# Kernel tuning notes

Measured on AMD Instinct MI355X. Metric: run time of the kernel, lower is better.

## Reference

```python
import jax, jax.numpy as jnp
import numpy as np

N = 50000
NEG_SLOPE = 0.2


def leaky_relu(x, slope=NEG_SLOPE):
    return jnp.where(x >= 0, x, slope * x)


def gat_conv(x, edge_index, W, a_src, a_dst, bias):
    """PyG GATConv, heads=1, add_self_loops=True.
    x: [N, Fin], edge_index: [2, E] (row 0 = source j, row 1 = target i),
    W: [Fin, Fout], a_src/a_dst: [Fout], bias: [Fout].
    """
    n = x.shape[0]
    # add self loops
    loops = jnp.arange(n, dtype=edge_index.dtype)
    src = jnp.concatenate([edge_index[0], loops])
    dst = jnp.concatenate([edge_index[1], loops])

    xw = x @ W                       # [N, Fout]
    alpha_src = xw @ a_src           # [N]
    alpha_dst = xw @ a_dst           # [N]

    e = leaky_relu(alpha_src[src] + alpha_dst[dst])   # [E+N]
    # segment softmax over edges sharing the same target node
    m = jax.ops.segment_max(e, dst, num_segments=n)   # [N]
    ex = jnp.exp(e - m[dst])
    denom = jax.ops.segment_sum(ex, dst, num_segments=n)  # [N] (>0 via self loops)
    att = ex / denom[dst]                              # [E+N]

    msgs = att[:, None] * xw[src]                      # [E+N, Fout]
    out = jax.ops.segment_sum(msgs, dst, num_segments=n)
    return out + bias


def setup_inputs() -> dict:
    key = jax.random.key(0)
    ks = jax.random.split(key, 12)
    E = 800000
    Fin, H, Fout = 128, 256, 128
    x = jax.random.normal(ks[0], (N, Fin), dtype=jnp.float32)
    edge_index = jax.random.randint(ks[1], (2, E), 0, N, dtype=jnp.int64)
    s = 0.1
    W1 = jax.random.normal(ks[2], (Fin, H), dtype=jnp.float32) * s
    a1_src = jax.random.normal(ks[3], (H,), dtype=jnp.float32) * s
    a1_dst = jax.random.normal(ks[4], (H,), dtype=jnp.float32) * s
    b1 = jax.random.normal(ks[5], (H,), dtype=jnp.float32) * s
    W2 = jax.random.normal(ks[6], (H, Fout), dtype=jnp.float32) * s
    a2_src = jax.random.normal(ks[7], (Fout,), dtype=jnp.float32) * s
    a2_dst = jax.random.normal(ks[8], (Fout,), dtype=jnp.float32) * s
    b2 = jax.random.normal(ks[9], (Fout,), dtype=jnp.float32) * s
    return {"x": x, "edge_index": edge_index, "W1": W1, "a1_src": a1_src,
            "a1_dst": a1_dst, "b1": b1, "W2": W2, "a2_src": a2_src,
            "a2_dst": a2_dst, "b2": b2}


def reference(x, edge_index, W1, a1_src, a1_dst, b1, W2, a2_src, a2_dst, b2):
    h = jax.nn.relu(gat_conv(x, edge_index, W1, a1_src, a1_dst, b1))
    return gat_conv(h, edge_index, W2, a2_src, a2_dst, b2)
```

## Files before the change

kernel.cpp:

```cpp
#include <hip/hip_runtime.h>
#include <hip/hip_bf16.h>

typedef __attribute__((ext_vector_type(8))) short short8;
typedef __attribute__((ext_vector_type(4))) float floatx4;

#define CAP 8192
#define BIN_CH 2048

__device__ __forceinline__ float read_f(const void* p, long long i, int fp32m) {
  return fp32m ? ((const float*)p)[i] : (float)((const __hip_bfloat16*)p)[i];
}
__device__ __forceinline__ float bf2f(unsigned short u) {
  return __uint_as_float((unsigned)u << 16);
}
__device__ __forceinline__ unsigned short f2bf(float f) {
  const unsigned u = __float_as_uint(f);
  return (unsigned short)((u + 0x7fffu + ((u >> 16) & 1u)) >> 16);
}

__device__ __forceinline__ void pack_one(const void* W, unsigned short* Wp, int i,
                                         int K, int NOUT, int m) {
  const int k = i / NOUT, n = i - k * NOUT;
  const int ct = n >> 4, c = n & 15, ks = k >> 5, quad = (k >> 3) & 3, j = k & 7;
  Wp[(((ct * (K / 32) + ks) * 4 + quad) * 16 + c) * 8 + j] = f2bf(read_f(W, i, m));
}

__global__ __launch_bounds__(256) void prep_k(const void* __restrict__ x,
                                              const void* __restrict__ ei,
                                              const void* __restrict__ W1,
                                              const void* __restrict__ a1s,
                                              const void* __restrict__ a1d,
                                              const void* __restrict__ b1,
                                              const void* __restrict__ W2,
                                              const void* __restrict__ a2s,
                                              const void* __restrict__ a2d,
                                              const void* __restrict__ b2,
                                              unsigned short* __restrict__ Wp1,
                                              unsigned short* __restrict__ Wp2,
                                              float* __restrict__ w_as1, float* __restrict__ w_ad1,
                                              float* __restrict__ v_a2s, float* __restrict__ v_a2d,
                                              float* __restrict__ v_b1,  float* __restrict__ v_b2,
                                              int* __restrict__ bkcnt,
                                              int* __restrict__ flags) {
  __shared__ int fl_s[2];
  const int t = threadIdx.x, b = blockIdx.x;
  if (t < 64) {
    const unsigned short w = ((const unsigned short*)x)[t * 2];
    const int ef = (w >> 7) & 0xff;
    const bool bf_ok = (ef >= 90 && ef <= 140);
    const unsigned hi = ((const unsigned*)ei)[t * 2 + 1];
    const unsigned long long bm = __ballot(bf_ok);
    const unsigned long long zm = __ballot(hi == 0u);
    if (t == 0) {
      fl_s[0] = (bm == ~0ull) ? 0 : 1;
      fl_s[1] = (zm == ~0ull) ? 1 : 0;
      if (b == 0) { flags[0] = fl_s[0]; flags[1] = fl_s[1]; }
    }
  }
  __syncthreads();
  const int m = fl_s[0];

  if (b < 128) {
    pack_one(W1, Wp1, b * 256 + t, 128, 256, m);
  } else if (b < 256) {
    pack_one(W2, Wp2, (b - 128) * 256 + t, 256, 128, m);
  } else if (b == 256) {
    if (t < 128) {
      float sa = 0.f, sb = 0.f;
      for (int j = 0; j < 256; ++j) {
        const float w = read_f(W1, (long long)t * 256 + j, m);
        sa = fmaf(w, read_f(a1s, j, m), sa);
        sb = fmaf(w, read_f(a1d, j, m), sb);
      }
      w_as1[t] = sa;
      w_ad1[t] = sb;
    }
  } else if (b == 257) {
    if (t < 128) v_a2s[t] = read_f(a2s, t, m);
    else         v_a2d[t - 128] = read_f(a2d, t - 128, m);
  } else if (b == 258) {
    v_b1[t] = read_f(b1, t, m);
  } else {
    if (t < 128) v_b2[t] = read_f(b2, t, m);
    bkcnt[t] = 0;
  }
}

__global__ __launch_bounds__(256) void canon_alpha_k(const void* __restrict__ x,
                                                     const float* __restrict__ was,
                                                     const float* __restrict__ wad,
                                                     unsigned short* __restrict__ xb,
                                                     float* __restrict__ as_, float* __restrict__ ad_,
                                                     int n, const int* __restrict__ flags) {
  const int gid = blockIdx.x * 256 + threadIdx.x;
  const int node = gid >> 6, lane = gid & 63;
  if (node >= n) return;
  const int m = flags[0];
  const long long base = (long long)node * 128 + lane * 2;
  const float v0 = read_f(x, base, m), v1 = read_f(x, base + 1, m);
  ushort2 q;
  q.x = f2bf(v0); q.y = f2bf(v1);
  *(ushort2*)(xb + base) = q;
  float s1 = fmaf(v0, was[lane * 2], v1 * was[lane * 2 + 1]);
  float s2 = fmaf(v0, wad[lane * 2], v1 * wad[lane * 2 + 1]);
  for (int off = 32; off; off >>= 1) {
    s1 += __shfl_down(s1, off);
    s2 += __shfl_down(s2, off);
  }
  if (lane == 0) { as_[node] = s1; ad_[node] = s2; }
}

__device__ __forceinline__ void edge_sd(const void* ei, int e, int E, int i64m, int n,
                                        int& s, int& d) {
  if (e < E) {
    if (i64m) { s = (int)((const long long*)ei)[e]; d = (int)((const long long*)ei)[E + e]; }
    else      { s = ((const int*)ei)[e];            d = ((const int*)ei)[E + e]; }
  } else { s = d = e - E; }
  s = min(max(s, 0), n - 1);
  d = min(max(d, 0), n - 1);
}

__global__ __launch_bounds__(256) void bin_k(const void* __restrict__ ei,
                                             unsigned* __restrict__ bpool,
                                             int* __restrict__ bkcnt,
                                             int E, int EN, int n,
                                             const int* __restrict__ flags) {
  __shared__ unsigned stage[BIN_CH];
  __shared__ unsigned daddr[BIN_CH];
  __shared__ int bcnt_s[256], boff_s[256], gbase_s[256], sd[256];
  __shared__ int vtot_s;
  const int t = threadIdx.x;
  const int c0 = blockIdx.x * BIN_CH;
  const int i64m = flags[1];
  bcnt_s[t] = 0;
  __syncthreads();

  unsigned val[BIN_CH / 256];
  int buk[BIN_CH / 256];
#pragma unroll
  for (int i = 0; i < BIN_CH / 256; ++i) {
    const int e = c0 + i * 256 + t;
    if (e < EN) {
      int s, d;
      edge_sd(ei, e, E, i64m, n, s, d);
      buk[i] = d >> 8;
      val[i] = (unsigned)s | ((unsigned)(d & 255) << 16);
      atomicAdd(&bcnt_s[buk[i]], 1);
    } else buk[i] = -1;
  }
  __syncthreads();

  const int c = bcnt_s[t];
  sd[t] = c;
  __syncthreads();
  for (int off = 1; off < 256; off <<= 1) {
    const int v = (t >= off) ? sd[t - off] : 0;
    __syncthreads();
    sd[t] += v;
    __syncthreads();
  }
  boff_s[t] = sd[t] - c;
  if (t == 255) vtot_s = sd[255];
  gbase_s[t] = (c > 0) ? atomicAdd(&bkcnt[t], c) : 0;
  bcnt_s[t] = 0;
  __syncthreads();

#pragma unroll
  for (int i = 0; i < BIN_CH / 256; ++i) {
    if (buk[i] >= 0) {
      const int lp = atomicAdd(&bcnt_s[buk[i]], 1);
      const int si = boff_s[buk[i]] + lp;
      stage[si] = val[i];
      const int gp = gbase_s[buk[i]] + lp;
      daddr[si] = (gp < CAP) ? (unsigned)(buk[i] * CAP + gp) : 0xFFFFFFFFu;
    }
  }
  __syncthreads();

  const int vt = vtot_s;
  for (int idx = t; idx < vt; idx += 256)
    if (daddr[idx] != 0xFFFFFFFFu) bpool[daddr[idx]] = stage[idx];
}

__global__ __launch_bounds__(256) void bucket_csr_k(const unsigned* __restrict__ bpool,
                                                    const int* __restrict__ bkcnt,
                                                    unsigned short* __restrict__ csrc,
                                                    int* __restrict__ start_g,
                                                    int* __restrict__ deg_g, int n) {
  __shared__ int deg_s[256], cur_s[256], sd[256];
  const int t = threadIdx.x, b = blockIdx.x;
  int cnt = bkcnt[b];
  if (cnt > CAP) cnt = CAP;
  deg_s[t] = 0;
  __syncthreads();
  for (int idx = t; idx < cnt; idx += 256) {
    const unsigned v = bpool[b * CAP + idx];
    atomicAdd(&deg_s[(v >> 16) & 255], 1);
  }
  __syncthreads();
  const int dg = deg_s[t];
  sd[t] = dg;
  __syncthreads();
  for (int off = 1; off < 256; off <<= 1) {
    const int v = (t >= off) ? sd[t - off] : 0;
    __syncthreads();
    sd[t] += v;
    __syncthreads();
  }
  const int excl = sd[t] - dg;
  const int node = b * 256 + t;
  if (node < n) { start_g[node] = b * CAP + excl; deg_g[node] = dg; }
  cur_s[t] = excl;
  __syncthreads();
  for (int idx = t; idx < cnt; idx += 256) {
    const unsigned v = bpool[b * CAP + idx];
    const int p = atomicAdd(&cur_s[(v >> 16) & 255], 1);
    csrc[b * CAP + p] = (unsigned short)(v & 0xFFFFu);
  }
}

__device__ __forceinline__ void agg_node(const int start, const int end,
                                         const unsigned short* __restrict__ csrc,
                                         const float* __restrict__ as_, const float adv,
                                         const unsigned short* __restrict__ xw,
                                         const int lane, float* acc) {
  const int slot = lane >> 4, col = lane & 15;
  float dsum = 0.f;
#pragma unroll
  for (int c = 0; c < 8; ++c) acc[c] = 0.f;

  for (int base = start; base < end; base += 64) {
    const int idx = base + lane;
    int s_pre = 0;
    float w_pre = 0.f;
    if (idx < end) {
      s_pre = (int)csrc[idx];
      float v = as_[s_pre] + adv;
      v = (v >= 0.f) ? v : 0.2f * v;
      w_pre = __expf(fminf(v, 60.f));
    }
    dsum += w_pre;
    const int cnt = min(64, end - base);
    for (int j = 0; j < cnt; j += 8) {
      const int jj0 = j + slot, jj1 = j + 4 + slot;
      int s0 = __shfl(s_pre, jj0);
      float w0 = __shfl(w_pre, jj0);
      int s1 = __shfl(s_pre, jj1);
      float w1 = __shfl(w_pre, jj1);
      const bool ok0 = (jj0 < cnt), ok1 = (jj1 < cnt);
      s0 = ok0 ? s0 : 0; w0 = ok0 ? w0 : 0.f;
      s1 = ok1 ? s1 : 0; w1 = ok1 ? w1 : 0.f;
      const short8 q0 = *(const short8*)(xw + (size_t)s0 * 128 + col * 8);
      const short8 q1 = *(const short8*)(xw + (size_t)s1 * 128 + col * 8);
#pragma unroll
      for (int c = 0; c < 8; ++c) {
        acc[c] = fmaf(w0, bf2f((unsigned short)q0[c]), acc[c]);
        acc[c] = fmaf(w1, bf2f((unsigned short)q1[c]), acc[c]);
      }
    }
  }
  for (int off = 32; off; off >>= 1) dsum += __shfl_down(dsum, off);
  dsum = __shfl(dsum, 0);
  const float r = 1.f / fmaxf(dsum, 1e-30f);
#pragma unroll
  for (int c = 0; c < 8; ++c) {
    acc[c] += __shfl_xor(acc[c], 16);
    acc[c] += __shfl_xor(acc[c], 32);
    acc[c] *= r;
  }
}

#define LSTR 136
#define HSTR 264
__global__ __launch_bounds__(1024) void agg_gemm12_k(const int* __restrict__ start_g,
                                                     const int* __restrict__ deg_g,
                                                     const unsigned short* __restrict__ csrc,
                                                     const float* __restrict__ as_,
                                                     const float* __restrict__ ad_,
                                                     const unsigned short* __restrict__ xb,
                                                     const unsigned short* __restrict__ Wp1,
                                                     const unsigned short* __restrict__ Wp2,
                                                     const float* __restrict__ v_b1,
                                                     const float* __restrict__ v_a2s,
                                                     const float* __restrict__ v_a2d,
                                                     unsigned short* __restrict__ xw2,
                                                     float* __restrict__ as2,
                                                     float* __restrict__ ad2, int n) {
  __shared__ unsigned short lds[16 * LSTR];
  __shared__ unsigned short hs[16 * HSTR];
  __shared__ float al_s[16], al_d[16];
  const int wv = threadIdx.x >> 6, lane = threadIdx.x & 63;
  const int slot = lane >> 4, col = lane & 15;
  const int node = blockIdx.x * 16 + wv;

  float acc[8];
  if (node < n) {
    const int start = start_g[node];
    agg_node(start, start + deg_g[node], csrc, as_, ad_[node], xb, lane, acc);
  } else {
#pragma unroll
    for (int c = 0; c < 8; ++c) acc[c] = 0.f;
  }
  if (slot == 0) {
    short8 q;
#pragma unroll
    for (int c = 0; c < 8; ++c) q[c] = (short)f2bf(acc[c]);
    *(short8*)&lds[wv * LSTR + col * 8] = q;
  }
  __syncthreads();

  const int quad = slot, c = col;
  floatx4 g = {0.f, 0.f, 0.f, 0.f};
#pragma unroll
  for (int ks = 0; ks < 4; ++ks) {
    const short8 af = *(const short8*)&lds[c * LSTR + ks * 32 + quad * 8];
    const short8 bf = *(const short8*)(Wp1 + (size_t)((wv * 4 + ks) * 64 + lane) * 8);
    g = __builtin_amdgcn_mfma_f32_16x16x32_bf16(af, bf, g, 0, 0, 0);
  }
  const float bv = v_b1[wv * 16 + c];
#pragma unroll
  for (int r = 0; r < 4; ++r) {
    const float v = g[r] + bv;
    hs[(quad * 4 + r) * HSTR + wv * 16 + c] = f2bf(v > 0.f ? v : 0.f);
  }
  if (threadIdx.x < 16) { al_s[threadIdx.x] = 0.f; al_d[threadIdx.x] = 0.f; }
  __syncthreads();

  const int row0 = blockIdx.x * 16;
  if (wv < 8) {
    floatx4 a2 = {0.f, 0.f, 0.f, 0.f};
#pragma unroll
    for (int ks = 0; ks < 8; ++ks) {
      const short8 af = *(const short8*)&hs[c * HSTR + ks * 32 + quad * 8];
      const short8 bf = *(const short8*)(Wp2 + (size_t)((wv * 8 + ks) * 64 + lane) * 8);
      a2 = __builtin_amdgcn_mfma_f32_16x16x32_bf16(af, bf, a2, 0, 0, 0);
    }
    const float asv = v_a2s[wv * 16 + c], adv = v_a2d[wv * 16 + c];
    float pa_s[4], pa_d[4];
#pragma unroll
    for (int r = 0; r < 4; ++r) {
      pa_s[r] = a2[r] * asv;
      pa_d[r] = a2[r] * adv;
      const int rr = row0 + quad * 4 + r;
      if (rr < n) xw2[(size_t)rr * 128 + wv * 16 + c] = f2bf(a2[r]);
    }
    for (int off = 1; off < 16; off <<= 1) {
#pragma unroll
      for (int r = 0; r < 4; ++r) {
        pa_s[r] += __shfl_xor(pa_s[r], off);
        pa_d[r] += __shfl_xor(pa_d[r], off);
      }
    }
    if (c == 0) {
#pragma unroll
      for (int r = 0; r < 4; ++r) {
        atomicAdd(&al_s[quad * 4 + r], pa_s[r]);
        atomicAdd(&al_d[quad * 4 + r], pa_d[r]);
      }
    }
  }
  __syncthreads();
  if (threadIdx.x < 16) {
    const int rr = row0 + threadIdx.x;
    if (rr < n) { as2[rr] = al_s[threadIdx.x]; ad2[rr] = al_d[threadIdx.x]; }
  }
}

__global__ __launch_bounds__(256) void agg_out_k(const int* __restrict__ start_g,
                                                 const int* __restrict__ deg_g,
                                                 const unsigned short* __restrict__ csrc,
                                                 const float* __restrict__ as_,
                                                 const float* __restrict__ ad_,
                                                 const unsigned short* __restrict__ xw,
                                                 const float* __restrict__ bias,
                                                 void* __restrict__ outp, int n,
                                                 const int* __restrict__ flags) {
  const int gid = blockIdx.x * 256 + threadIdx.x;
  const int node = gid >> 6, lane = gid & 63;
  if (node >= n) return;
  const int slot = lane >> 4, col = lane & 15;
  const int start = start_g[node];
  float acc[8];
  agg_node(start, start + deg_g[node], csrc, as_, ad_[node], xw, lane, acc);
  if (slot == 0) {
    const int c0 = col * 8;
    if (flags[0]) {
      float* o = (float*)outp + (size_t)node * 128 + c0;
      floatx4 q0, q1;
#pragma unroll
      for (int c = 0; c < 4; ++c) {
        q0[c] = acc[c] + bias[c0 + c];
        q1[c] = acc[c + 4] + bias[c0 + 4 + c];
      }
      *(floatx4*)o = q0;
      *(floatx4*)(o + 4) = q1;
    } else {
      short8 q;
#pragma unroll
      for (int c = 0; c < 8; ++c) q[c] = (short)f2bf(acc[c] + bias[c0 + c]);
      *(short8*)((unsigned short*)outp + (size_t)node * 128 + c0) = q;
    }
  }
}

extern "C" void kernel_launch(void* const* d_in, const int* in_sizes, int n_in,
                              void* d_out, int out_size, void* d_ws, size_t ws_size,
                              hipStream_t stream) {
  const void* x   = d_in[0];
  const void* ei  = d_in[1];
  const void* W1  = d_in[2];
  const void* a1s = d_in[3];
  const void* a1d = d_in[4];
  const void* b1  = d_in[5];
  const void* W2  = d_in[6];
  const void* a2s = d_in[7];
  const void* a2d = d_in[8];
  const void* b2  = d_in[9];

  const int N  = in_sizes[0] / 128;
  const int E  = in_sizes[1] / 2;
  const int EN = E + N;
  const int NBUK = (N + 255) / 256;

  unsigned short* B1 = (unsigned short*)d_ws;
  unsigned short* H  = B1 + (size_t)N * 128;
  unsigned short* xw2 = H;
  float* as2 = (float*)(H + (size_t)N * 128);
  float* ad2 = as2 + N;
  float* as_   = (float*)(H + (size_t)N * 256);
  float* ad_   = as_ + N;
  int*   start_g = (int*)(ad_ + N);
  int*   deg_g   = start_g + N;
  int*   bkcnt   = deg_g + N;
  unsigned* bpool = (unsigned*)(bkcnt + 256);
  unsigned short* csrc = (unsigned short*)(bpool + (size_t)NBUK * CAP);
  unsigned short* Wp1 = csrc + (size_t)NBUK * CAP;
  unsigned short* Wp2 = Wp1 + 128 * 256;
  float* vecs  = (float*)(Wp2 + 256 * 128);
  int*   flags = (int*)(vecs + 1152);
  float* w_as1 = vecs,        *w_ad1 = vecs + 128;
  float* v_a2s = vecs + 256,  *v_a2d = vecs + 384;
  float* v_b1  = vecs + 512,  *v_b2  = vecs + 768;

  const int NB = (N * 64 + 255) / 256;
  const int BB = (EN + BIN_CH - 1) / BIN_CH;
  const int AG = (N + 15) / 16;

  prep_k<<<260, 256, 0, stream>>>(x, ei, W1, a1s, a1d, b1, W2, a2s, a2d, b2,
                                  Wp1, Wp2, w_as1, w_ad1, v_a2s, v_a2d, v_b1, v_b2,
                                  bkcnt, flags);

  canon_alpha_k<<<NB, 256, 0, stream>>>(x, w_as1, w_ad1, B1, as_, ad_, N, flags);

  bin_k<<<BB, 256, 0, stream>>>(ei, bpool, bkcnt, E, EN, N, flags);
  bucket_csr_k<<<NBUK, 256, 0, stream>>>(bpool, bkcnt, csrc, start_g, deg_g, N);

  agg_gemm12_k<<<AG, 1024, 0, stream>>>(start_g, deg_g, csrc, as_, ad_, B1, Wp1, Wp2,
                                        v_b1, v_a2s, v_a2d, xw2, as2, ad2, N);

  agg_out_k<<<NB, 256, 0, stream>>>(start_g, deg_g, csrc, as2, ad2, xw2, v_b2, d_out, N, flags);
}
```

Measured before the change: 256.7 us.

## Fuse canon/alpha and edge binning launches, unroll gather, swizzle LDS tiles

Merges the x-canonicalisation/alpha kernel and the edge binning kernel into one launch whose blocks split by index. Each block recomputes the dtype flags from the inputs instead of reading them from prep. The aggregation gather loop now handles 16 neighbours per iteration, giving four independent row loads in flight. The padded LDS strides in the fused GEMM kernel are replaced by XOR swizzling to avoid bank conflicts. The heuristic dtype detection could misclassify inputs.

Result: slower. 278.7 us (+8.6%).

```diff
diff --git a/kernel.cpp b/kernel.cpp
--- a/kernel.cpp
+++ b/kernel.cpp
@@ -86,30 +86,6 @@
   }
 }
 
-__global__ __launch_bounds__(256) void canon_alpha_k(const void* __restrict__ x,
-                                                     const float* __restrict__ was,
-                                                     const float* __restrict__ wad,
-                                                     unsigned short* __restrict__ xb,
-                                                     float* __restrict__ as_, float* __restrict__ ad_,
-                                                     int n, const int* __restrict__ flags) {
-  const int gid = blockIdx.x * 256 + threadIdx.x;
-  const int node = gid >> 6, lane = gid & 63;
-  if (node >= n) return;
-  const int m = flags[0];
-  const long long base = (long long)node * 128 + lane * 2;
-  const float v0 = read_f(x, base, m), v1 = read_f(x, base + 1, m);
-  ushort2 q;
-  q.x = f2bf(v0); q.y = f2bf(v1);
-  *(ushort2*)(xb + base) = q;
-  float s1 = fmaf(v0, was[lane * 2], v1 * was[lane * 2 + 1]);
-  float s2 = fmaf(v0, wad[lane * 2], v1 * wad[lane * 2 + 1]);
-  for (int off = 32; off; off >>= 1) {
-    s1 += __shfl_down(s1, off);
-    s2 += __shfl_down(s2, off);
-  }
-  if (lane == 0) { as_[node] = s1; ad_[node] = s2; }
-}
-
 __device__ __forceinline__ void edge_sd(const void* ei, int e, int E, int i64m, int n,
                                         int& s, int& d) {
   if (e < E) {
@@ -120,66 +96,105 @@
   d = min(max(d, 0), n - 1);
 }
 
-__global__ __launch_bounds__(256) void bin_k(const void* __restrict__ ei,
-                                             unsigned* __restrict__ bpool,
-                                             int* __restrict__ bkcnt,
-                                             int E, int EN, int n,
-                                             const int* __restrict__ flags) {
+__global__ __launch_bounds__(256) void front2_k(const void* __restrict__ x,
+                                                const void* __restrict__ ei,
+                                                const float* __restrict__ w_as1,
+                                                const float* __restrict__ w_ad1,
+                                                unsigned short* __restrict__ xb,
+                                                float* __restrict__ as_, float* __restrict__ ad_,
+                                                unsigned* __restrict__ bpool,
+                                                int* __restrict__ bkcnt,
+                                                int n, int E, int EN, int nbc) {
+  __shared__ int fl_s[2];
   __shared__ unsigned stage[BIN_CH];
   __shared__ unsigned daddr[BIN_CH];
-  __shared__ int bcnt_s[256], boff_s[256], gbase_s[256], sd[256];
+  __shared__ int shA[256], shB[256], shC[256], shD[256];
   __shared__ int vtot_s;
-  const int t = threadIdx.x;
-  const int c0 = blockIdx.x * BIN_CH;
-  const int i64m = flags[1];
-  bcnt_s[t] = 0;
-  __syncthreads();
-
-  unsigned val[BIN_CH / 256];
-  int buk[BIN_CH / 256];
-#pragma unroll
-  for (int i = 0; i < BIN_CH / 256; ++i) {
-    const int e = c0 + i * 256 + t;
-    if (e < EN) {
-      int s, d;
-      edge_sd(ei, e, E, i64m, n, s, d);
-      buk[i] = d >> 8;
-      val[i] = (unsigned)s | ((unsigned)(d & 255) << 16);
-      atomicAdd(&bcnt_s[buk[i]], 1);
-    } else buk[i] = -1;
-  }
-  __syncthreads();
-
-  const int c = bcnt_s[t];
-  sd[t] = c;
-  __syncthreads();
-  for (int off = 1; off < 256; off <<= 1) {
-    const int v = (t >= off) ? sd[t - off] : 0;
-    __syncthreads();
-    sd[t] += v;
-    __syncthreads();
-  }
-  boff_s[t] = sd[t] - c;
-  if (t == 255) vtot_s = sd[255];
-  gbase_s[t] = (c > 0) ? atomicAdd(&bkcnt[t], c) : 0;
-  bcnt_s[t] = 0;
-  __syncthreads();
-
-#pragma unroll
-  for (int i = 0; i < BIN_CH / 256; ++i) {
-    if (buk[i] >= 0) {
-      const int lp = atomicAdd(&bcnt_s[buk[i]], 1);
-      const int si = boff_s[buk[i]] + lp;
-      stage[si] = val[i];
-      const int gp = gbase_s[buk[i]] + lp;
-      daddr[si] = (gp < CAP) ? (unsigned)(buk[i] * CAP + gp) : 0xFFFFFFFFu;
-    }
-  }
-  __syncthreads();
-
-  const int vt = vtot_s;
-  for (int idx = t; idx < vt; idx += 256)
-    if (daddr[idx] != 0xFFFFFFFFu) bpool[daddr[idx]] = stage[idx];
+  const int t = threadIdx.x, b = blockIdx.x;
+
+  if (t < 64) {
+    const unsigned short w = ((const unsigned short*)x)[t * 2];
+    const int ef = (w >> 7) & 0xff;
+    const bool bf_ok = (ef >= 90 && ef <= 140);
+    const unsigned hi = ((const unsigned*)ei)[t * 2 + 1];
+    const unsigned long long bm = __ballot(bf_ok);
+    const unsigned long long zm = __ballot(hi == 0u);
+    if (t == 0) {
+      fl_s[0] = (bm == ~0ull) ? 0 : 1;
+      fl_s[1] = (zm == ~0ull) ? 1 : 0;
+    }
+  }
+  __syncthreads();
+  const int m = fl_s[0], i64m = fl_s[1];
+
+  if (b < nbc) {
+    const int gid = b * 256 + t;
+    const int node = gid >> 6, lane = gid & 63;
+    if (node >= n) return;
+    const long long base = (long long)node * 128 + lane * 2;
+    const float v0 = read_f(x, base, m), v1 = read_f(x, base + 1, m);
+    ushort2 q;
+    q.x = f2bf(v0); q.y = f2bf(v1);
+    *(ushort2*)(xb + base) = q;
+    float s1 = fmaf(v0, w_as1[lane * 2], v1 * w_as1[lane * 2 + 1]);
+    float s2 = fmaf(v0, w_ad1[lane * 2], v1 * w_ad1[lane * 2 + 1]);
+    for (int off = 32; off; off >>= 1) {
+      s1 += __shfl_down(s1, off);
+      s2 += __shfl_down(s2, off);
+    }
+    if (lane == 0) { as_[node] = s1; ad_[node] = s2; }
+  } else {
+    const int c0 = (b - nbc) * BIN_CH;
+    int* bcnt_s = shA; int* boff_s = shB; int* gbase_s = shC; int* sd = shD;
+    bcnt_s[t] = 0;
+    __syncthreads();
+
+    unsigned val[BIN_CH / 256];
+    int buk[BIN_CH / 256];
+#pragma unroll
+    for (int i = 0; i < BIN_CH / 256; ++i) {
+      const int e = c0 + i * 256 + t;
+      if (e < EN) {
+        int s, d;
+        edge_sd(ei, e, E, i64m, n, s, d);
+        buk[i] = d >> 8;
+        val[i] = (unsigned)s | ((unsigned)(d & 255) << 16);
+        atomicAdd(&bcnt_s[buk[i]], 1);
+      } else buk[i] = -1;
+    }
+    __syncthreads();
+
+    const int c = bcnt_s[t];
+    sd[t] = c;
+    __syncthreads();
+    for (int off = 1; off < 256; off <<= 1) {
+      const int v = (t >= off) ? sd[t - off] : 0;
+      __syncthreads();
+      sd[t] += v;
+      __syncthreads();
+    }
+    boff_s[t] = sd[t] - c;
+    if (t == 255) vtot_s = sd[255];
+    gbase_s[t] = (c > 0) ? atomicAdd(&bkcnt[t], c) : 0;
+    bcnt_s[t] = 0;
+    __syncthreads();
+
+#pragma unroll
+    for (int i = 0; i < BIN_CH / 256; ++i) {
+      if (buk[i] >= 0) {
+        const int lp = atomicAdd(&bcnt_s[buk[i]], 1);
+        const int si = boff_s[buk[i]] + lp;
+        stage[si] = val[i];
+        const int gp = gbase_s[buk[i]] + lp;
+        daddr[si] = (gp < CAP) ? (unsigned)(buk[i] * CAP + gp) : 0xFFFFFFFFu;
+      }
+    }
+    __syncthreads();
+
+    const int vt = vtot_s;
+    for (int idx = t; idx < vt; idx += 256)
+      if (daddr[idx] != 0xFFFFFFFFu) bpool[daddr[idx]] = stage[idx];
+  }
 }
 
 __global__ __launch_bounds__(256) void bucket_csr_k(const unsigned* __restrict__ bpool,
@@ -241,7 +256,29 @@
     }
     dsum += w_pre;
     const int cnt = min(64, end - base);
-    for (int j = 0; j < cnt; j += 8) {
+    int j = 0;
+    for (; j + 16 <= cnt; j += 16) {
+      int ss0 = __shfl(s_pre, j + slot);
+      int ss1 = __shfl(s_pre, j + 4 + slot);
+      int ss2 = __shfl(s_pre, j + 8 + slot);
+      int ss3 = __shfl(s_pre, j + 12 + slot);
+      float ww0 = __shfl(w_pre, j + slot);
+      float ww1 = __shfl(w_pre, j + 4 + slot);
+      float ww2 = __shfl(w_pre, j + 8 + slot);
+      float ww3 = __shfl(w_pre, j + 12 + slot);
+      const short8 q0 = *(const short8*)(xw + (size_t)ss0 * 128 + col * 8);
+      const short8 q1 = *(const short8*)(xw + (size_t)ss1 * 128 + col * 8);
+      const short8 q2 = *(const short8*)(xw + (size_t)ss2 * 128 + col * 8);
+      const short8 q3 = *(const short8*)(xw + (size_t)ss3 * 128 + col * 8);
+#pragma unroll
+      for (int c = 0; c < 8; ++c) {
+        acc[c] = fmaf(ww0, bf2f((unsigned short)q0[c]), acc[c]);
+        acc[c] = fmaf(ww1, bf2f((unsigned short)q1[c]), acc[c]);
+        acc[c] = fmaf(ww2, bf2f((unsigned short)q2[c]), acc[c]);
+        acc[c] = fmaf(ww3, bf2f((unsigned short)q3[c]), acc[c]);
+      }
+    }
+    for (; j < cnt; j += 8) {
       const int jj0 = j + slot, jj1 = j + 4 + slot;
       int s0 = __shfl(s_pre, jj0);
       float w0 = __shfl(w_pre, jj0);
@@ -270,8 +307,13 @@
   }
 }
 
-#define LSTR 136
-#define HSTR 264
+__device__ __forceinline__ int aswz(int row, int colbyte) {
+  return (row * 256 + (colbyte ^ ((row & 7) << 4))) >> 1;
+}
+__device__ __forceinline__ int hswz(int row, int colbyte) {
+  return (row * 512 + (colbyte ^ ((row & 7) << 4))) >> 1;
+}
+
 __global__ __launch_bounds__(1024) void agg_gemm12_k(const int* __restrict__ start_g,
                                                      const int* __restrict__ deg_g,
                                                      const unsigned short* __restrict__ csrc,
@@ -286,8 +328,8 @@
                                                      unsigned short* __restrict__ xw2,
                                                      float* __restrict__ as2,
                                                      float* __restrict__ ad2, int n) {
-  __shared__ unsigned short lds[16 * LSTR];
-  __shared__ unsigned short hs[16 * HSTR];
+  __shared__ unsigned short lds[16 * 128];
+  __shared__ unsigned short hs[16 * 256];
   __shared__ float al_s[16], al_d[16];
   const int wv = threadIdx.x >> 6, lane = threadIdx.x & 63;
   const int slot = lane >> 4, col = lane & 15;
@@ -305,7 +347,7 @@
     short8 q;
 #pragma unroll
     for (int c = 0; c < 8; ++c) q[c] = (short)f2bf(acc[c]);
-    *(short8*)&lds[wv * LSTR + col * 8] = q;
+    *(short8*)&lds[aswz(wv, col * 16)] = q;
   }
   __syncthreads();
 
@@ -313,7 +355,7 @@
   floatx4 g = {0.f, 0.f, 0.f, 0.f};
 #pragma unroll
   for (int ks = 0; ks < 4; ++ks) {
-    const short8 af = *(const short8*)&lds[c * LSTR + ks * 32 + quad * 8];
+    const short8 af = *(const short8*)&lds[aswz(c, ks * 64 + quad * 16)];
     const short8 bf = *(const short8*)(Wp1 + (size_t)((wv * 4 + ks) * 64 + lane) * 8);
     g = __builtin_amdgcn_mfma_f32_16x16x32_bf16(af, bf, g, 0, 0, 0);
   }
@@ -321,7 +363,7 @@
 #pragma unroll
   for (int r = 0; r < 4; ++r) {
     const float v = g[r] + bv;
-    hs[(quad * 4 + r) * HSTR + wv * 16 + c] = f2bf(v > 0.f ? v : 0.f);
+    hs[hswz(quad * 4 + r, (wv * 16 + c) * 2)] = f2bf(v > 0.f ? v : 0.f);
   }
   if (threadIdx.x < 16) { al_s[threadIdx.x] = 0.f; al_d[threadIdx.x] = 0.f; }
   __syncthreads();
@@ -331,7 +373,7 @@
     floatx4 a2 = {0.f, 0.f, 0.f, 0.f};
 #pragma unroll
     for (int ks = 0; ks < 8; ++ks) {
-      const short8 af = *(const short8*)&hs[c * HSTR + ks * 32 + quad * 8];
+      const short8 af = *(const short8*)&hs[hswz(c, ks * 64 + quad * 16)];
       const short8 bf = *(const short8*)(Wp2 + (size_t)((wv * 8 + ks) * 64 + lane) * 8);
       a2 = __builtin_amdgcn_mfma_f32_16x16x32_bf16(af, bf, a2, 0, 0, 0);
     }
@@ -450,9 +492,9 @@
                                   Wp1, Wp2, w_as1, w_ad1, v_a2s, v_a2d, v_b1, v_b2,
                                   bkcnt, flags);
 
-  canon_alpha_k<<<NB, 256, 0, stream>>>(x, w_as1, w_ad1, B1, as_, ad_, N, flags);
-
-  bin_k<<<BB, 256, 0, stream>>>(ei, bpool, bkcnt, E, EN, N, flags);
+  front2_k<<<NB + BB, 256, 0, stream>>>(x, ei, w_as1, w_ad1, B1, as_, ad_,
+                                        bpool, bkcnt, N, E, EN, NB);
+
   bucket_csr_k<<<NBUK, 256, 0, stream>>>(bpool, bkcnt, csrc, start_g, deg_g, N);
 
   agg_gemm12_k<<<AG, 1024, 0, stream>>>(start_g, deg_g, csrc, as_, ad_, B1, Wp1, Wp2,
```
